# Kernel tuning notes

Measured on AMD Instinct MI355X. Metric: run time of the kernel, lower is better.

## Reference

```python
import jax, jax.numpy as jnp
import numpy as np

DIM = 1024
HEADS = 16
HEAD_DIM = 64
INNER = HEADS * HEAD_DIM  # 1024
SCALE = 8.0
LN_EPS = 1e-5
NORM_EPS = 1e-12  # F.normalize default eps


def layer_norm(x, g, b):
    m = jnp.mean(x, axis=-1, keepdims=True)
    v = jnp.mean((x - m) ** 2, axis=-1, keepdims=True)
    return (x - m) * jax.lax.rsqrt(v + LN_EPS) * g + b


def l2_normalize(x):
    n = jnp.sqrt(jnp.sum(x * x, axis=-1, keepdims=True))
    return x / jnp.maximum(n, NORM_EPS)


def setup_inputs() -> dict:
    key = jax.random.key(0)
    ks = jax.random.split(key, 8)
    B, N, T = 4, 4096, 256
    s = 0.02
    return {
        "x": jax.random.normal(ks[0], (B, N, DIM), jnp.float32),
        "context": jax.random.normal(ks[1], (B, T, DIM), jnp.float32),
        "Wq": jax.random.normal(ks[2], (DIM, INNER), jnp.float32) * s,
        "Wkv": jax.random.normal(ks[3], (DIM, 2 * INNER), jnp.float32) * s,
        "Wo": jax.random.normal(ks[4], (INNER, DIM), jnp.float32) * s,
        "null_kv": jax.random.normal(ks[5], (2, HEAD_DIM), jnp.float32),
        "q_scale": jnp.ones((HEAD_DIM,), jnp.float32),
        "k_scale": jnp.ones((HEAD_DIM,), jnp.float32),
        "ln_in_g": jnp.ones((DIM,), jnp.float32),
        "ln_in_b": jnp.zeros((DIM,), jnp.float32),
        "ln_ctx_g": jnp.ones((DIM,), jnp.float32),
        "ln_ctx_b": jnp.zeros((DIM,), jnp.float32),
        "ln_out_g": jnp.ones((DIM,), jnp.float32),
        "ln_out_b": jnp.zeros((DIM,), jnp.float32),
    }


def reference(x, context, Wq, Wkv, Wo, null_kv, q_scale, k_scale,
              ln_in_g, ln_in_b, ln_ctx_g, ln_ctx_b, ln_out_g, ln_out_b):
    B, N, _ = x.shape
    T = context.shape[1]
    xn = layer_norm(x, ln_in_g, ln_in_b)
    cn = layer_norm(context, ln_ctx_g, ln_ctx_b)
    q = xn @ Wq                      # [B, N, INNER]
    kv = cn @ Wkv                    # [B, T, 2*INNER]
    k, v = jnp.split(kv, 2, axis=-1)
    # split heads: b s (h d) -> b h s d
    def split_heads(t):
        b, s, _ = t.shape
        return t.reshape(b, s, HEADS, HEAD_DIM).transpose(0, 2, 1, 3)
    q, k, v = split_heads(q), split_heads(k), split_heads(v)
    # null kv token appended along kv-seq dim
    nk = jnp.broadcast_to(null_kv[0], (B, HEADS, 1, HEAD_DIM))
    nv = jnp.broadcast_to(null_kv[1], (B, HEADS, 1, HEAD_DIM))
    k = jnp.concatenate([k, nk], axis=2)   # [B, H, T+1, D]
    v = jnp.concatenate([v, nv], axis=2)
    q = l2_normalize(q) * q_scale
    k = l2_normalize(k) * k_scale
    scores = jnp.einsum('bhid,bhkd->bhik', q, k) * SCALE
    attn = jax.nn.softmax(scores, axis=-1)
    out = jnp.einsum('bhik,bhkd->bhid', attn, v)   # [B, H, N, D]
    out = out.transpose(0, 2, 1, 3).reshape(B, N, INNER)
    out = out @ Wo
    return layer_norm(out, ln_out_g, ln_out_b)
```

## Files before the change

kernel.cpp:

```cpp
#include <hip/hip_runtime.h>
#include <cstdint>
#include <cstddef>

typedef _Float16 f16;
typedef _Float16 f16x4 __attribute__((ext_vector_type(4)));
typedef _Float16 f16x8 __attribute__((ext_vector_type(8)));
typedef float f32x4 __attribute__((ext_vector_type(4)));
typedef __fp16 h16x2 __attribute__((ext_vector_type(2)));

#define DIM 1024
#define B_ 4
#define N_ 4096
#define TKP 288
#define SCALE_ 8.0f
#define LOG2E 1.4426950408889634f

__device__ __forceinline__ void gload_lds16(const void* g, void* l) {
  __builtin_amdgcn_global_load_lds(
      reinterpret_cast<const __attribute__((address_space(1))) uint32_t*>(
          reinterpret_cast<uintptr_t>(g)),
      reinterpret_cast<__attribute__((address_space(3))) uint32_t*>(
          reinterpret_cast<uintptr_t>(l)),
      16, 0, 0);
}

__global__ void transpose_all_kernel(const float* __restrict__ Wq,
                                     const float* __restrict__ Wkv,
                                     const float* __restrict__ Wo,
                                     f16* __restrict__ wqT, f16* __restrict__ wkvT,
                                     f16* __restrict__ woT) {
  int bid = blockIdx.x;
  const float* W; f16* WT; int K = 1024, N; int tb;
  if (bid < 1024)      { W = Wq;  WT = wqT;  N = 1024; tb = bid; }
  else if (bid < 3072) { W = Wkv; WT = wkvT; N = 2048; tb = bid - 1024; }
  else                 { W = Wo;  WT = woT;  N = 1024; tb = bid - 3072; }
  __shared__ float tile[32][33];
  int nt = N >> 5;
  int tk = tb / nt, tn = tb % nt;
  int tx = threadIdx.x & 31, ty = threadIdx.x >> 5;
#pragma unroll
  for (int p = 0; p < 32; p += 8)
    tile[ty + p][tx] = W[(size_t)(tk * 32 + ty + p) * N + tn * 32 + tx];
  __syncthreads();
#pragma unroll
  for (int p = 0; p < 32; p += 8)
    WT[(size_t)(tn * 32 + ty + p) * K + tk * 32 + tx] = (f16)tile[tx][ty + p];
}

__device__ __forceinline__ void ln_row_f16out(const float4 v, const float* g,
                                              const float* bb, int t, f16* outrow) {
  float s = v.x + v.y + v.z + v.w;
  float ss = v.x * v.x + v.y * v.y + v.z * v.z + v.w * v.w;
#pragma unroll
  for (int m = 1; m < 64; m <<= 1) { s += __shfl_xor(s, m); ss += __shfl_xor(ss, m); }
  __shared__ float red[8];
  int w = t >> 6;
  if ((t & 63) == 0) { red[w * 2] = s; red[w * 2 + 1] = ss; }
  __syncthreads();
  s = red[0] + red[2] + red[4] + red[6];
  ss = red[1] + red[3] + red[5] + red[7];
  float mean = s * (1.0f / DIM);
  float var = ss * (1.0f / DIM) - mean * mean;
  float rstd = rsqrtf(var + 1e-5f);
  float4 gv = ((const float4*)g)[t];
  float4 bv = ((const float4*)bb)[t];
  f16x4 h = {(f16)((v.x - mean) * rstd * gv.x + bv.x),
             (f16)((v.y - mean) * rstd * gv.y + bv.y),
             (f16)((v.z - mean) * rstd * gv.z + bv.z),
             (f16)((v.w - mean) * rstd * gv.w + bv.w)};
  *(f16x4*)(outrow + t * 4) = h;
}

__global__ void ln_xc_kernel(const float* __restrict__ x, const float* __restrict__ ctx,
                             const float* __restrict__ gx, const float* __restrict__ bx,
                             const float* __restrict__ gc, const float* __restrict__ bc,
                             f16* __restrict__ xn, f16* __restrict__ cn) {
  int row = blockIdx.x;
  int t = threadIdx.x;
  const float* in; const float* g; const float* bb; f16* out; int r;
  if (row < 16384) { in = x; g = gx; bb = bx; out = xn; r = row; }
  else             { in = ctx; g = gc; bb = bc; out = cn; r = row - 16384; }
  float4 v = ((const float4*)(in + (size_t)r * DIM))[t];
  ln_row_f16out(v, g, bb, t, out + (size_t)r * DIM);
}

__global__ void ln_out_kernel(const f16* __restrict__ in, const float* __restrict__ g,
                              const float* __restrict__ bb, float* __restrict__ out) {
  int row = blockIdx.x;
  int t = threadIdx.x;
  f16x4 h = ((const f16x4*)(in + (size_t)row * DIM))[t];
  float4 v = {(float)h[0], (float)h[1], (float)h[2], (float)h[3]};
  float s = v.x + v.y + v.z + v.w;
  float ss = v.x * v.x + v.y * v.y + v.z * v.z + v.w * v.w;
#pragma unroll
  for (int m = 1; m < 64; m <<= 1) { s += __shfl_xor(s, m); ss += __shfl_xor(ss, m); }
  __shared__ float red[8];
  int w = t >> 6;
  if ((t & 63) == 0) { red[w * 2] = s; red[w * 2 + 1] = ss; }
  __syncthreads();
  s = red[0] + red[2] + red[4] + red[6];
  ss = red[1] + red[3] + red[5] + red[7];
  float mean = s * (1.0f / DIM);
  float var = ss * (1.0f / DIM) - mean * mean;
  float rstd = rsqrtf(var + 1e-5f);
  float4 gv = ((const float4*)g)[t];
  float4 bv = ((const float4*)bb)[t];
  float4 o = {(v.x - mean) * rstd * gv.x + bv.x, (v.y - mean) * rstd * gv.y + bv.y,
              (v.z - mean) * rstd * gv.z + bv.z, (v.w - mean) * rstd * gv.w + bv.w};
  *(float4*)(out + (size_t)row * DIM + t * 4) = o;
}

template <bool OUT_F32>
__global__ __launch_bounds__(256, 2) void gemm_nt_kernel(
    const f16* __restrict__ A, const f16* __restrict__ Bt, void* __restrict__ C,
    int M, int N, int K) {
  __shared__ f16 As[128 * 64];
  __shared__ f16 Bs[128 * 64];
  int nb = N >> 7;
  int cpx = gridDim.x >> 3;
  int wg = ((int)blockIdx.x & 7) * cpx + ((int)blockIdx.x >> 3);
  int bm = wg / nb, bn = wg % nb;
  int t = threadIdx.x;
  int lane = t & 63, w = t >> 6;
  int wm = w >> 1, wn = w & 1;
  int r16 = lane & 15, g4 = lane >> 4;
  f32x4 acc[4][4] = {};
  for (int k0 = 0; k0 < K; k0 += 64) {
#pragma unroll
    for (int i = 0; i < 4; ++i) {
      int li = i * 256 + t;
      int r = li >> 3, c = li & 7;
      int kc = ((c ^ (r & 7)) << 3);
      gload_lds16(A + (size_t)(bm * 128 + r) * K + k0 + kc, (char*)As + li * 16);
      gload_lds16(Bt + (size_t)(bn * 128 + r) * K + k0 + kc, (char*)Bs + li * 16);
    }
    __syncthreads();
#pragma unroll
    for (int ks = 0; ks < 2; ++ks) {
      f16x8 af[4], bf[4];
#pragma unroll
      for (int mi = 0; mi < 4; ++mi) {
        int r = wm * 64 + mi * 16 + r16;
        int cidx = ks * 4 + g4;
        af[mi] = *(const f16x8*)(As + r * 64 + ((cidx ^ (r & 7)) << 3));
      }
#pragma unroll
      for (int ni = 0; ni < 4; ++ni) {
        int r = wn * 64 + ni * 16 + r16;
        int cidx = ks * 4 + g4;
        bf[ni] = *(const f16x8*)(Bs + r * 64 + ((cidx ^ (r & 7)) << 3));
      }
#pragma unroll
      for (int mi = 0; mi < 4; ++mi)
#pragma unroll
        for (int ni = 0; ni < 4; ++ni)
          acc[mi][ni] = __builtin_amdgcn_mfma_f32_16x16x32_f16(af[mi], bf[ni],
                                                               acc[mi][ni], 0, 0, 0);
    }
    __syncthreads();
  }
  int cr0 = bm * 128 + wm * 64;
  int cc = bn * 128 + wn * 64 + r16;
#pragma unroll
  for (int mi = 0; mi < 4; ++mi)
#pragma unroll
    for (int ni = 0; ni < 4; ++ni)
#pragma unroll
      for (int j = 0; j < 4; ++j) {
        int row = cr0 + mi * 16 + g4 * 4 + j;
        int col = cc + ni * 16;
        if constexpr (OUT_F32)
          ((float*)C)[(size_t)row * N + col] = acc[mi][ni][j];
        else
          ((f16*)C)[(size_t)row * N + col] = (f16)acc[mi][ni][j];
      }
}

__global__ void prep_kv_kernel(const f16* __restrict__ kv, const float* __restrict__ nullkv,
                               const float* __restrict__ ks, f16* __restrict__ Karr,
                               f16* __restrict__ Varr) {
  int bh = blockIdx.x;
  int b = bh >> 4, h = bh & 15;
  int t = threadIdx.x;
  __shared__ f16 vt[256][65];
  const f16* krow = kv + (size_t)(b * 256 + t) * 2048 + h * 64;
  const f16* vrow = krow + 1024;
  f16x8 kd[8];
  float ss = 0.0f;
#pragma unroll
  for (int i = 0; i < 8; ++i) {
    kd[i] = *(const f16x8*)(krow + i * 8);
#pragma unroll
    for (int j = 0; j < 8; ++j) { float x = (float)kd[i][j]; ss += x * x; }
  }
  float inv = 1.0f / fmaxf(sqrtf(ss), 1e-12f);
  f16* kout = Karr + ((size_t)bh * TKP + t) * 64;
#pragma unroll
  for (int i = 0; i < 8; ++i) {
    f16x8 o;
#pragma unroll
    for (int j = 0; j < 8; ++j) o[j] = (f16)((float)kd[i][j] * inv * ks[i * 8 + j]);
    *(f16x8*)(kout + i * 8) = o;
  }
#pragma unroll
  for (int i = 0; i < 8; ++i) {
    f16x8 vv = *(const f16x8*)(vrow + i * 8);
#pragma unroll
    for (int j = 0; j < 8; ++j) vt[t][i * 8 + j] = vv[j];
  }
  if (t < 32) {
    f16* kr = Karr + ((size_t)bh * TKP + 256 + t) * 64;
    if (t == 0) {
      float ssn = 0.0f;
      for (int d = 0; d < 64; ++d) ssn += nullkv[d] * nullkv[d];
      float invn = 1.0f / fmaxf(sqrtf(ssn), 1e-12f);
      for (int d = 0; d < 64; ++d) kr[d] = (f16)(nullkv[d] * invn * ks[d]);
    } else {
      for (int d = 0; d < 64; ++d) kr[d] = (f16)0.0f;
    }
  }
  __syncthreads();
  f16* vbase = Varr + (size_t)bh * 64 * TKP;
  int pcol = (t & ~31) | (((t & 15) << 1) | ((t >> 4) & 1));
  for (int d = 0; d < 64; ++d) vbase[(size_t)d * TKP + pcol] = vt[t][d];
#pragma unroll
  for (int i = 0; i < 8; ++i) {
    int idx = i * 256 + t;
    int d = idx >> 5, key = 256 + (idx & 31);
    vbase[(size_t)d * TKP + key] = (key == 256) ? (f16)nullkv[64 + d] : (f16)0.0f;
  }
}

__global__ __launch_bounds__(256, 4) void attn_kernel(
    const f16* __restrict__ Q, const f16* __restrict__ Karr,
    const f16* __restrict__ Varr, const float* __restrict__ qs,
    const float* __restrict__ ksc, f16* __restrict__ O) {
  int wgid = ((int)blockIdx.x & 7) * 256 + ((int)blockIdx.x >> 3);
  int qb = wgid & 31, bh = wgid >> 5;
  int b = bh >> 4, h = bh & 15;
  int t = threadIdx.x, lane = t & 63, w = t >> 6;
  int r16 = lane & 15, g4 = lane >> 4;
  int row0 = b * N_ + qb * 128 + w * 32;
  int col0 = h * 64;
  const f16* Kp = Karr + (size_t)bh * TKP * 64;
  const f16* Vp = Varr + (size_t)bh * 64 * TKP;
  __shared__ f16 Ks[2][32 * 64];
  __shared__ f16 Vs[2][64 * 32];
  __shared__ f16 Plds[4][32 * 40];
  f16* Pw = &Plds[w][0];
  int krow_s = t >> 3;
  int kc_s = (t & 7) ^ (krow_s & 7);
  int vrow_s = t >> 2;
  int vc_s = (t & 3) ^ ((vrow_s >> 1) & 3);
  float mq = fabsf(qs[lane]), mk = fabsf(ksc[lane]);
#pragma unroll
  for (int m = 1; m < 64; m <<= 1) {
    mq = fmaxf(mq, __shfl_xor(mq, m));
    mk = fmaxf(mk, __shfl_xor(mk, m));
  }
  const float c1 = SCALE_ * LOG2E;
  const float c2 = SCALE_ * mq * mk * LOG2E;
  gload_lds16(Kp + (size_t)krow_s * 64 + kc_s * 8, (char*)Ks[0] + t * 16);
  gload_lds16(Vp + (size_t)vrow_s * TKP + 0 + vc_s * 8, (char*)Vs[0] + t * 16);
  float qsv[2][8];
#pragma unroll
  for (int kdh = 0; kdh < 2; ++kdh)
#pragma unroll
    for (int i = 0; i < 8; ++i) qsv[kdh][i] = qs[kdh * 32 + g4 * 8 + i];
  f16x8 qf[2][2];
#pragma unroll
  for (int mi = 0; mi < 2; ++mi) {
    float f[2][8];
    float ssq = 0.0f;
#pragma unroll
    for (int kdh = 0; kdh < 2; ++kdh) {
      f16x8 v = *(const f16x8*)(Q + (size_t)(row0 + mi * 16 + r16) * DIM +
                                col0 + kdh * 32 + g4 * 8);
#pragma unroll
      for (int i = 0; i < 8; ++i) { f[kdh][i] = (float)v[i]; ssq += f[kdh][i] * f[kdh][i]; }
    }
    ssq += __shfl_xor(ssq, 16);
    ssq += __shfl_xor(ssq, 32);
    float inv = 1.0f / fmaxf(sqrtf(ssq), 1e-12f);
#pragma unroll
    for (int kdh = 0; kdh < 2; ++kdh) {
      f16x8 o;
#pragma unroll
      for (int i = 0; i < 8; ++i) o[i] = (f16)(f[kdh][i] * inv * qsv[kdh][i]);
      qf[mi][kdh] = o;
    }
  }
  f32x4 o[2][4] = {};
  float part[2][4] = {};
  const h16x2 ones2 = {(__fp16)1.0f, (__fp16)1.0f};
  __syncthreads();
#pragma unroll
  for (int kt = 0; kt < 9; ++kt) {
    const int cur = kt & 1;
    const int key0 = kt * 32;
    if (kt < 8) {
      const int nxt = key0 + 32;
      gload_lds16(Kp + (size_t)(nxt + krow_s) * 64 + kc_s * 8,
                  (char*)Ks[cur ^ 1] + t * 16);
      gload_lds16(Vp + (size_t)vrow_s * TKP + nxt + vc_s * 8,
                  (char*)Vs[cur ^ 1] + t * 16);
    }
    f16x8 kf[2][2];
#pragma unroll
    for (int ni = 0; ni < 2; ++ni)
#pragma unroll
      for (int kdh = 0; kdh < 2; ++kdh) {
        int row = ni * 16 + r16;
        int cidx = kdh * 4 + g4;
        kf[ni][kdh] = *(const f16x8*)(Ks[cur] + row * 64 + ((cidx ^ (row & 7)) << 3));
      }
    f32x4 s[2][2] = {};
    __builtin_amdgcn_s_setprio(1);
#pragma unroll
    for (int kdh = 0; kdh < 2; ++kdh)
#pragma unroll
      for (int mi = 0; mi < 2; ++mi)
#pragma unroll
        for (int ni = 0; ni < 2; ++ni)
          s[mi][ni] = __builtin_amdgcn_mfma_f32_16x16x32_f16(qf[mi][kdh], kf[ni][kdh],
                                                             s[mi][ni], 0, 0, 0);
    __builtin_amdgcn_s_setprio(0);
    float nb0 = (key0 + r16 <= 256) ? -c2 : -(c2 + 128.0f);
    float nb1 = (key0 + 16 + r16 <= 256) ? -c2 : -(c2 + 128.0f);
#pragma unroll
    for (int mi = 0; mi < 2; ++mi) {
#pragma unroll
      for (int j = 0; j < 4; ++j) {
        float p0 = __builtin_amdgcn_exp2f(s[mi][0][j] * c1 + nb0);
        float p1 = __builtin_amdgcn_exp2f(s[mi][1][j] * c1 + nb1);
        h16x2 pk = __builtin_amdgcn_cvt_pkrtz(p0, p1);
        part[mi][j] = __builtin_amdgcn_fdot2(pk, ones2, part[mi][j], false);
        int prow = mi * 16 + g4 * 4 + j;
        ((uint32_t*)(Pw + prow * 40))[r16] = __builtin_bit_cast(uint32_t, pk);
      }
    }
    f16x8 vf[4];
#pragma unroll
    for (int nd = 0; nd < 4; ++nd) {
      int row = nd * 16 + r16;
      int slot = g4 ^ ((row >> 1) & 3);
      vf[nd] = *(const f16x8*)(Vs[cur] + row * 32 + (slot << 3));
    }
    __builtin_amdgcn_s_setprio(1);
#pragma unroll
    for (int mi = 0; mi < 2; ++mi) {
      f16x8 pa = *(const f16x8*)(Pw + (mi * 16 + r16) * 40 + g4 * 8);
#pragma unroll
      for (int nd = 0; nd < 4; ++nd)
        o[mi][nd] = __builtin_amdgcn_mfma_f32_16x16x32_f16(pa, vf[nd], o[mi][nd], 0, 0, 0);
    }
    __builtin_amdgcn_s_setprio(0);
    __syncthreads();
  }
#pragma unroll
  for (int mi = 0; mi < 2; ++mi)
#pragma unroll
    for (int j = 0; j < 4; ++j) {
      float v = part[mi][j];
      v += __shfl_xor(v, 1); v += __shfl_xor(v, 2);
      v += __shfl_xor(v, 4); v += __shfl_xor(v, 8);
      part[mi][j] = v;
    }
#pragma unroll
  for (int mi = 0; mi < 2; ++mi)
#pragma unroll
    for (int j = 0; j < 4; ++j) {
      float inv = 1.0f / part[mi][j];
      int row = row0 + mi * 16 + g4 * 4 + j;
#pragma unroll
      for (int nd = 0; nd < 4; ++nd)
        O[(size_t)row * DIM + col0 + nd * 16 + r16] = (f16)(o[mi][nd][j] * inv);
    }
}

extern "C" void kernel_launch(void* const* d_in, const int* in_sizes, int n_in,
                              void* d_out, int out_size, void* d_ws, size_t ws_size,
                              hipStream_t stream) {
  const float* x      = (const float*)d_in[0];
  const float* ctx    = (const float*)d_in[1];
  const float* Wq     = (const float*)d_in[2];
  const float* Wkv    = (const float*)d_in[3];
  const float* Wo     = (const float*)d_in[4];
  const float* nullkv = (const float*)d_in[5];
  const float* qs     = (const float*)d_in[6];
  const float* ks     = (const float*)d_in[7];
  const float* g_in   = (const float*)d_in[8];
  const float* b_in   = (const float*)d_in[9];
  const float* g_ctx  = (const float*)d_in[10];
  const float* b_ctx  = (const float*)d_in[11];
  const float* g_out  = (const float*)d_in[12];
  const float* b_out  = (const float*)d_in[13];

  char* ws = (char*)d_ws;
  const size_t MB = 1ull << 20;
  f16* wqT   = (f16*)(ws + 0);
  f16* wkvT  = (f16*)(ws + 2 * MB);
  f16* woT   = (f16*)(ws + 6 * MB);
  f16* karr  = (f16*)(ws + 8 * MB);
  f16* varr  = (f16*)(ws + 11 * MB);
  f16* cn    = (f16*)(ws + 14 * MB);
  f16* kvb   = (f16*)(ws + 16 * MB);
  f16* xn    = (f16*)(ws + 20 * MB);
  f16* q_raw = (f16*)(ws + 52 * MB);
  f16* aout  = (f16*)(ws + 20 * MB);
  f16* out2h = (f16*)(ws + 52 * MB);

  transpose_all_kernel<<<4096, 256, 0, stream>>>(Wq, Wkv, Wo, wqT, wkvT, woT);

  ln_xc_kernel<<<16384 + 1024, 256, 0, stream>>>(x, ctx, g_in, b_in, g_ctx, b_ctx,
                                                 xn, cn);

  gemm_nt_kernel<false><<<(16384 / 128) * (1024 / 128), 256, 0, stream>>>(
      xn, wqT, (void*)q_raw, 16384, 1024, 1024);
  gemm_nt_kernel<false><<<(1024 / 128) * (2048 / 128), 256, 0, stream>>>(
      cn, wkvT, (void*)kvb, 1024, 2048, 1024);

  prep_kv_kernel<<<64, 256, 0, stream>>>(kvb, nullkv, ks, karr, varr);

  attn_kernel<<<2048, 256, 0, stream>>>(q_raw, karr, varr, qs, ks, aout);

  gemm_nt_kernel<false><<<(16384 / 128) * (1024 / 128), 256, 0, stream>>>(
      aout, woT, (void*)out2h, 16384, 1024, 1024);

  ln_out_kernel<<<16384, 256, 0, stream>>>(out2h, g_out, b_out, (float*)d_out);
}
```

Measured before the change: 330.2 us.

## Fuse Q l2-normalize into Q GEMM epilogue and triple-buffer K/V in attention

The Q projection GEMM epilogue now computes each row's per-head L2 norm from the fp32 accumulators with lane shuffles, then applies q_scale before writing fp16. The attention kernel therefore loads the normalized Q directly instead of normalizing it. Attention also moves from double to triple buffering of the K/V LDS tiles, prefetching two tiles ahead with explicit vmcnt waits and raw barriers in place of __syncthreads. Normalizing from fp32 accumulators also changes precision slightly, and the extra LDS may reduce occupancy.

```diff
diff --git a/kernel.cpp b/kernel.cpp
--- a/kernel.cpp
+++ b/kernel.cpp
@@ -110,10 +110,10 @@
   *(float4*)(out + (size_t)row * DIM + t * 4) = o;
 }
 
-template <bool OUT_F32>
+template <bool NORMQ>
 __global__ __launch_bounds__(256, 2) void gemm_nt_kernel(
-    const f16* __restrict__ A, const f16* __restrict__ Bt, void* __restrict__ C,
-    int M, int N, int K) {
+    const f16* __restrict__ A, const f16* __restrict__ Bt, f16* __restrict__ C,
+    const float* __restrict__ qs, int M, int N, int K) {
   __shared__ f16 As[128 * 64];
   __shared__ f16 Bs[128 * 64];
   int nb = N >> 7;
@@ -161,19 +161,32 @@
   }
   int cr0 = bm * 128 + wm * 64;
   int cc = bn * 128 + wn * 64 + r16;
+  float qsv[4];
+  if constexpr (NORMQ) {
+#pragma unroll
+    for (int ni = 0; ni < 4; ++ni) qsv[ni] = qs[ni * 16 + r16];
+  }
 #pragma unroll
   for (int mi = 0; mi < 4; ++mi)
 #pragma unroll
-    for (int ni = 0; ni < 4; ++ni)
-#pragma unroll
-      for (int j = 0; j < 4; ++j) {
-        int row = cr0 + mi * 16 + g4 * 4 + j;
-        int col = cc + ni * 16;
-        if constexpr (OUT_F32)
-          ((float*)C)[(size_t)row * N + col] = acc[mi][ni][j];
-        else
-          ((f16*)C)[(size_t)row * N + col] = (f16)acc[mi][ni][j];
-      }
+    for (int j = 0; j < 4; ++j) {
+      float inv = 1.0f;
+      if constexpr (NORMQ) {
+        float ssq = 0.0f;
+#pragma unroll
+        for (int ni = 0; ni < 4; ++ni) ssq += acc[mi][ni][j] * acc[mi][ni][j];
+        ssq += __shfl_xor(ssq, 1); ssq += __shfl_xor(ssq, 2);
+        ssq += __shfl_xor(ssq, 4); ssq += __shfl_xor(ssq, 8);
+        inv = 1.0f / fmaxf(sqrtf(ssq), 1e-12f);
+      }
+      int row = cr0 + mi * 16 + g4 * 4 + j;
+#pragma unroll
+      for (int ni = 0; ni < 4; ++ni) {
+        float v = acc[mi][ni][j];
+        if constexpr (NORMQ) v = v * inv * qsv[ni];
+        C[(size_t)row * N + cc + ni * 16] = (f16)v;
+      }
+    }
 }
 
 __global__ void prep_kv_kernel(const f16* __restrict__ kv, const float* __restrict__ nullkv,
@@ -244,14 +257,18 @@
   int col0 = h * 64;
   const f16* Kp = Karr + (size_t)bh * TKP * 64;
   const f16* Vp = Varr + (size_t)bh * 64 * TKP;
-  __shared__ f16 Ks[2][32 * 64];
-  __shared__ f16 Vs[2][64 * 32];
+  __shared__ f16 Ks[3][32 * 64];
+  __shared__ f16 Vs[3][64 * 32];
   __shared__ f16 Plds[4][32 * 40];
   f16* Pw = &Plds[w][0];
   int krow_s = t >> 3;
   int kc_s = (t & 7) ^ (krow_s & 7);
   int vrow_s = t >> 2;
   int vc_s = (t & 3) ^ ((vrow_s >> 1) & 3);
+  gload_lds16(Kp + (size_t)krow_s * 64 + kc_s * 8, (char*)Ks[0] + t * 16);
+  gload_lds16(Vp + (size_t)vrow_s * TKP + 0 + vc_s * 8, (char*)Vs[0] + t * 16);
+  gload_lds16(Kp + (size_t)(32 + krow_s) * 64 + kc_s * 8, (char*)Ks[1] + t * 16);
+  gload_lds16(Vp + (size_t)vrow_s * TKP + 32 + vc_s * 8, (char*)Vs[1] + t * 16);
   float mq = fabsf(qs[lane]), mk = fabsf(ksc[lane]);
 #pragma unroll
   for (int m = 1; m < 64; m <<= 1) {
@@ -260,50 +277,30 @@
   }
   const float c1 = SCALE_ * LOG2E;
   const float c2 = SCALE_ * mq * mk * LOG2E;
-  gload_lds16(Kp + (size_t)krow_s * 64 + kc_s * 8, (char*)Ks[0] + t * 16);
-  gload_lds16(Vp + (size_t)vrow_s * TKP + 0 + vc_s * 8, (char*)Vs[0] + t * 16);
-  float qsv[2][8];
-#pragma unroll
-  for (int kdh = 0; kdh < 2; ++kdh)
-#pragma unroll
-    for (int i = 0; i < 8; ++i) qsv[kdh][i] = qs[kdh * 32 + g4 * 8 + i];
   f16x8 qf[2][2];
 #pragma unroll
-  for (int mi = 0; mi < 2; ++mi) {
-    float f[2][8];
-    float ssq = 0.0f;
-#pragma unroll
-    for (int kdh = 0; kdh < 2; ++kdh) {
-      f16x8 v = *(const f16x8*)(Q + (size_t)(row0 + mi * 16 + r16) * DIM +
-                                col0 + kdh * 32 + g4 * 8);
-#pragma unroll
-      for (int i = 0; i < 8; ++i) { f[kdh][i] = (float)v[i]; ssq += f[kdh][i] * f[kdh][i]; }
-    }
-    ssq += __shfl_xor(ssq, 16);
-    ssq += __shfl_xor(ssq, 32);
-    float inv = 1.0f / fmaxf(sqrtf(ssq), 1e-12f);
-#pragma unroll
-    for (int kdh = 0; kdh < 2; ++kdh) {
-      f16x8 o;
-#pragma unroll
-      for (int i = 0; i < 8; ++i) o[i] = (f16)(f[kdh][i] * inv * qsv[kdh][i]);
-      qf[mi][kdh] = o;
-    }
-  }
+  for (int mi = 0; mi < 2; ++mi)
+#pragma unroll
+    for (int kdh = 0; kdh < 2; ++kdh)
+      qf[mi][kdh] = *(const f16x8*)(Q + (size_t)(row0 + mi * 16 + r16) * DIM +
+                                    col0 + kdh * 32 + g4 * 8);
   f32x4 o[2][4] = {};
   float part[2][4] = {};
   const h16x2 ones2 = {(__fp16)1.0f, (__fp16)1.0f};
-  __syncthreads();
+  asm volatile("s_waitcnt vmcnt(2)" ::: "memory");
+  __builtin_amdgcn_s_barrier();
+  __builtin_amdgcn_sched_barrier(0);
 #pragma unroll
   for (int kt = 0; kt < 9; ++kt) {
-    const int cur = kt & 1;
+    const int cur = kt % 3;
     const int key0 = kt * 32;
-    if (kt < 8) {
-      const int nxt = key0 + 32;
+    if (kt < 7) {
+      const int nxt = key0 + 64;
+      const int nbuf = (kt + 2) % 3;
       gload_lds16(Kp + (size_t)(nxt + krow_s) * 64 + kc_s * 8,
-                  (char*)Ks[cur ^ 1] + t * 16);
+                  (char*)Ks[nbuf] + t * 16);
       gload_lds16(Vp + (size_t)vrow_s * TKP + nxt + vc_s * 8,
-                  (char*)Vs[cur ^ 1] + t * 16);
+                  (char*)Vs[nbuf] + t * 16);
     }
     f16x8 kf[2][2];
 #pragma unroll
@@ -355,7 +352,15 @@
         o[mi][nd] = __builtin_amdgcn_mfma_f32_16x16x32_f16(pa, vf[nd], o[mi][nd], 0, 0, 0);
     }
     __builtin_amdgcn_s_setprio(0);
-    __syncthreads();
+    if (kt < 7) {
+      asm volatile("s_waitcnt vmcnt(2)" ::: "memory");
+      __builtin_amdgcn_s_barrier();
+      __builtin_amdgcn_sched_barrier(0);
+    } else if (kt == 7) {
+      asm volatile("s_waitcnt vmcnt(0)" ::: "memory");
+      __builtin_amdgcn_s_barrier();
+      __builtin_amdgcn_sched_barrier(0);
+    }
   }
 #pragma unroll
   for (int mi = 0; mi < 2; ++mi)
@@ -406,7 +411,7 @@
   f16* cn    = (f16*)(ws + 14 * MB);
   f16* kvb   = (f16*)(ws + 16 * MB);
   f16* xn    = (f16*)(ws + 20 * MB);
-  f16* q_raw = (f16*)(ws + 52 * MB);
+  f16* qn    = (f16*)(ws + 52 * MB);
   f16* aout  = (f16*)(ws + 20 * MB);
   f16* out2h = (f16*)(ws + 52 * MB);
 
@@ -415,17 +420,17 @@
   ln_xc_kernel<<<16384 + 1024, 256, 0, stream>>>(x, ctx, g_in, b_in, g_ctx, b_ctx,
                                                  xn, cn);
 
+  gemm_nt_kernel<true><<<(16384 / 128) * (1024 / 128), 256, 0, stream>>>(
+      xn, wqT, qn, qs, 16384, 1024, 1024);
+  gemm_nt_kernel<false><<<(1024 / 128) * (2048 / 128), 256, 0, stream>>>(
+      cn, wkvT, kvb, nullptr, 1024, 2048, 1024);
+
+  prep_kv_kernel<<<64, 256, 0, stream>>>(kvb, nullkv, ks, karr, varr);
+
+  attn_kernel<<<2048, 256, 0, stream>>>(qn, karr, varr, qs, ks, aout);
+
   gemm_nt_kernel<false><<<(16384 / 128) * (1024 / 128), 256, 0, stream>>>(
-      xn, wqT, (void*)q_raw, 16384, 1024, 1024);
-  gemm_nt_kernel<false><<<(1024 / 128) * (2048 / 128), 256, 0, stream>>>(
-      cn, wkvT, (void*)kvb, 1024, 2048, 1024);
-
-  prep_kv_kernel<<<64, 256, 0, stream>>>(kvb, nullkv, ks, karr, varr);
-
-  attn_kernel<<<2048, 256, 0, stream>>>(q_raw, karr, varr, qs, ks, aout);
-
-  gemm_nt_kernel<false><<<(16384 / 128) * (1024 / 128), 256, 0, stream>>>(
-      aout, woT, (void*)out2h, 16384, 1024, 1024);
+      aout, woT, out2h, nullptr, 16384, 1024, 1024);
 
   ln_out_kernel<<<16384, 256, 0, stream>>>(out2h, g_out, b_out, (float*)d_out);
 }
```

New measurement: 326.0 us. Within noise of the previous version (-1.3%).
